# Optimization experiments

Measured on AMD Instinct MI355X. Metric: run time of the kernel, lower is better.

Reference implementation:

```python
import jax, jax.numpy as jnp
import numpy as np

B, S, H = 2, 2048, 1024
NH, HD = 16, 64
WIN = 256
EPS = 1e-5


def _layernorm(x, g, b):
    # normalize over last dim (head_dim)
    m = jnp.mean(x, axis=-1, keepdims=True)
    v = jnp.mean((x - m) ** 2, axis=-1, keepdims=True)
    return (x - m) * jax.lax.rsqrt(v + EPS) * g + b


def setup_inputs() -> dict:
    key = jax.random.key(0)
    ks = jax.random.split(key, 6)
    scale = 1.0 / np.sqrt(2.0 * H)  # ~ xavier_uniform with gain 1/sqrt(2)
    inp = {
        "x": jax.random.normal(ks[0], (B, S, H), dtype=jnp.float32),
        "Wq": jax.random.normal(ks[1], (H, H), dtype=jnp.float32) * scale,
        "bq": jnp.zeros((H,), jnp.float32),
        "Wk": jax.random.normal(ks[2], (H, H), dtype=jnp.float32) * scale,
        "bk": jnp.zeros((H,), jnp.float32),
        "Wv": jax.random.normal(ks[3], (H, H), dtype=jnp.float32) * scale,
        "bv": jnp.zeros((H,), jnp.float32),
        "Wo": jax.random.normal(ks[4], (H, H), dtype=jnp.float32) * scale,
        "bo": jnp.zeros((H,), jnp.float32),
        "ln_q_w": jnp.ones((HD,), jnp.float32),
        "ln_q_b": jnp.zeros((HD,), jnp.float32),
        "ln_k_w": jnp.ones((HD,), jnp.float32),
        "ln_k_b": jnp.zeros((HD,), jnp.float32),
    }
    return inp


def reference(x, Wq, bq, Wk, bk, Wv, bv, Wo, bo, ln_q_w, ln_q_b, ln_k_w, ln_k_b):
    b, s, _ = x.shape
    # projections (torch Linear: x @ W.T + b)
    q = (x @ Wq.T + bq).reshape(b, s, NH, HD)
    k = (x @ Wk.T + bk).reshape(b, s, NH, HD)
    v = (x @ Wv.T + bv).reshape(b, s, NH, HD)
    # QK layernorm over head_dim
    q = _layernorm(q, ln_q_w, ln_q_b)
    k = _layernorm(k, ln_k_w, ln_k_b)
    # scores [b, h, s, s]
    scores = jnp.einsum("bqhd,bkhd->bhqk", q, k) / np.sqrt(HD).astype(np.float32)
    i = jnp.arange(s)[:, None]
    j = jnp.arange(s)[None, :]
    mask = (j <= i) & (i - j <= WIN)
    scores = jnp.where(mask[None, None], scores, -jnp.inf)
    probs = jax.nn.softmax(scores, axis=-1)
    out = jnp.einsum("bhqk,bkhd->bqhd", probs, v).reshape(b, s, NH * HD)
    return out @ Wo.T + bo
```

## Files before the change

kernel.cpp:

```cpp
#include <hip/hip_runtime.h>
#include <hip/hip_bf16.h>
#include <cstdint>

typedef __hip_bfloat16 bf16;
typedef __attribute__((ext_vector_type(8))) short s16x8;
typedef __attribute__((ext_vector_type(4))) float f32x4;

#define NB_B 2
#define NB_S 2048
#define NB_H 1024
#define NB_NH 16
#define NB_HD 64
#define NB_WIN 256
#define NTOK 4096

static __device__ __forceinline__ unsigned pack_bf16(float a, float b) {
    bf16 ta = __float2bfloat16(a), tb = __float2bfloat16(b);
    return (unsigned)*(unsigned short*)&ta | ((unsigned)*(unsigned short*)&tb << 16);
}
static __device__ __forceinline__ unsigned short bf16u(float a) {
    bf16 t = __float2bfloat16(a);
    return *(unsigned short*)&t;
}

#define VMCNT(n) asm volatile("s_waitcnt vmcnt(" #n ")" ::: "memory")
#define SBAR __builtin_amdgcn_s_barrier()

__global__ void k_castall(const float* __restrict__ x, const float* __restrict__ Wq,
                          const float* __restrict__ Wk, const float* __restrict__ Wv,
                          const float* __restrict__ Wo,
                          bf16* __restrict__ xb, bf16* __restrict__ wqkvb,
                          bf16* __restrict__ wob) {
    int idx = blockIdx.x * blockDim.x + threadIdx.x;
    const float* in; bf16* out; int i;
    if (idx < 1048576)        { in = x;  out = xb;              i = idx * 4; }
    else if (idx < 1310720)   { in = Wq; out = wqkvb;           i = (idx - 1048576) * 4; }
    else if (idx < 1572864)   { in = Wk; out = wqkvb + 1048576; i = (idx - 1310720) * 4; }
    else if (idx < 1835008)   { in = Wv; out = wqkvb + 2097152; i = (idx - 1572864) * 4; }
    else                      { in = Wo; out = wob;             i = (idx - 1835008) * 4; }
    const float4 v = *(const float4*)(in + i);
    ushort4 u;
    u.x = bf16u(v.x); u.y = bf16u(v.y); u.z = bf16u(v.z); u.w = bf16u(v.w);
    *(ushort4*)((unsigned short*)out + i) = u;
}

#define G2_STAGE(AD, BD, KT)                                                         \
    do {                                                                             \
        _Pragma("unroll")                                                            \
        for (int it_ = 0; it_ < 4; ++it_) {                                          \
            int c_ = it_ * 512 + tid;                                                \
            int row_ = c_ >> 3, pc_ = c_ & 7;                                        \
            int col_ = ((pc_ ^ (row_ & 7)) << 3);                                    \
            __builtin_amdgcn_global_load_lds(                                        \
                (const __attribute__((address_space(1))) void*)(Ap + (size_t)(m0 + row_) * 1024 + (KT) + col_), \
                (__attribute__((address_space(3))) void*)((AD) + c_ * 8), 16, 0, 0); \
            __builtin_amdgcn_global_load_lds(                                        \
                (const __attribute__((address_space(1))) void*)(Bp + (size_t)(n0 + row_) * 1024 + (KT) + col_), \
                (__attribute__((address_space(3))) void*)((BD) + c_ * 8), 16, 0, 0); \
        }                                                                            \
        __builtin_amdgcn_sched_barrier(0);                                           \
    } while (0)

#define G2_COMPUTE(AS, BS)                                                           \
    do {                                                                             \
        _Pragma("unroll")                                                            \
        for (int kk_ = 0; kk_ < 2; ++kk_) {                                          \
            const int rchunk_ = (((kk_ << 2) + g) ^ (q & 7)) << 3;                   \
            s16x8 af_[8], bf_[4];                                                    \
            _Pragma("unroll")                                                        \
            for (int mi_ = 0; mi_ < 8; ++mi_)                                        \
                af_[mi_] = *(const s16x8*)&(AS)[(wr * 128 + mi_ * 16 + q) * 64 + rchunk_]; \
            _Pragma("unroll")                                                        \
            for (int ni_ = 0; ni_ < 4; ++ni_)                                        \
                bf_[ni_] = *(const s16x8*)&(BS)[(wc * 64 + ni_ * 16 + q) * 64 + rchunk_]; \
            __builtin_amdgcn_s_setprio(1);                                           \
            _Pragma("unroll")                                                        \
            for (int mi_ = 0; mi_ < 8; ++mi_)                                        \
                _Pragma("unroll")                                                    \
                for (int ni_ = 0; ni_ < 4; ++ni_)                                    \
                    acc[mi_][ni_] = __builtin_amdgcn_mfma_f32_16x16x32_bf16(         \
                        af_[mi_], bf_[ni_], acc[mi_][ni_], 0, 0, 0);                 \
            __builtin_amdgcn_s_setprio(0);                                           \
        }                                                                            \
    } while (0)

#define G2_MAINLOOP                                                                  \
    G2_STAGE(As0, Bs0, 0);                                                           \
    G2_STAGE(As1, Bs1, 64);                                                          \
    for (int i_ = 0; i_ < 7; ++i_) {                                                 \
        const int kt_ = i_ * 128;                                                    \
        VMCNT(8); SBAR;                                                              \
        G2_COMPUTE(As0, Bs0);                                                        \
        SBAR;                                                                        \
        G2_STAGE(As0, Bs0, kt_ + 128);                                               \
        VMCNT(8); SBAR;                                                              \
        G2_COMPUTE(As1, Bs1);                                                        \
        SBAR;                                                                        \
        G2_STAGE(As1, Bs1, kt_ + 192);                                               \
    }                                                                                \
    VMCNT(8); SBAR;                                                                  \
    G2_COMPUTE(As0, Bs0);                                                            \
    VMCNT(0); SBAR;                                                                  \
    G2_COMPUTE(As1, Bs1)

__global__ __launch_bounds__(512, 2) void k_gemm_qkv(const bf16* __restrict__ Ap,
                                                  const bf16* __restrict__ Bp,
                                                  const float* __restrict__ bq,
                                                  const float* __restrict__ bk,
                                                  const float* __restrict__ bv,
                                                  const float* __restrict__ lqw,
                                                  const float* __restrict__ lqb,
                                                  const float* __restrict__ lkw,
                                                  const float* __restrict__ lkb,
                                                  bf16* __restrict__ qbuf,
                                                  bf16* __restrict__ kbuf,
                                                  bf16* __restrict__ vtb) {
    __shared__ bf16 As0[256 * 64], As1[256 * 64];
    __shared__ bf16 Bs0[256 * 64], Bs1[256 * 64];
    const int tid = threadIdx.x;
    const int lane = tid & 63;
    const int wid = tid >> 6;
    const int wr = wid >> 2, wc = wid & 3;

    const int orig = blockIdx.y * gridDim.x + blockIdx.x;
    const int wk = (orig & 7) * 24 + (orig >> 3);
    const int m0 = (wk / 12) * 256, n0 = (wk % 12) * 256;

    const int g = lane >> 4, q = lane & 15;

    f32x4 acc[8][4] = {};

    G2_MAINLOOP;

    const int col0 = n0 + wc * 64;
    const int hh = col0 >> 6;
    const int csub = col0 & 1023;
    const float* bias = (hh < 16) ? bq : (hh < 32) ? bk : bv;

    float bcol[4];
#pragma unroll
    for (int ni = 0; ni < 4; ++ni) bcol[ni] = bias[csub + ni * 16 + q];
#pragma unroll
    for (int mi = 0; mi < 8; ++mi)
#pragma unroll
        for (int ni = 0; ni < 4; ++ni)
#pragma unroll
            for (int r = 0; r < 4; ++r) acc[mi][ni][r] += bcol[ni];

    if (hh < 32) {
        const float* gwa = (hh < 16) ? lqw : lkw;
        const float* gba = (hh < 16) ? lqb : lkb;
        float gam[4], bet[4];
#pragma unroll
        for (int ni = 0; ni < 4; ++ni) {
            gam[ni] = gwa[ni * 16 + q];
            bet[ni] = gba[ni * 16 + q];
        }
        bf16* outp = (hh < 16) ? qbuf : kbuf;
#pragma unroll
        for (int mi = 0; mi < 8; ++mi)
#pragma unroll
            for (int r = 0; r < 4; ++r) {
                float s1 = acc[mi][0][r] + acc[mi][1][r] + acc[mi][2][r] + acc[mi][3][r];
                float s2 = acc[mi][0][r] * acc[mi][0][r] + acc[mi][1][r] * acc[mi][1][r]
                         + acc[mi][2][r] * acc[mi][2][r] + acc[mi][3][r] * acc[mi][3][r];
#pragma unroll
                for (int mm = 1; mm < 16; mm <<= 1) {
                    s1 += __shfl_xor(s1, mm, 64);
                    s2 += __shfl_xor(s2, mm, 64);
                }
                float mean = s1 * (1.f / 64.f);
                float var = s2 * (1.f / 64.f) - mean * mean;
                float rs = rsqrtf(var + 1e-5f);
                int token = m0 + wr * 128 + mi * 16 + g * 4 + r;
#pragma unroll
                for (int ni = 0; ni < 4; ++ni) {
                    float y = (acc[mi][ni][r] - mean) * rs * gam[ni] + bet[ni];
                    outp[(size_t)token * 1024 + csub + ni * 16 + q] = __float2bfloat16(y);
                }
            }
    } else {
        const int b = m0 >> 11;
        const int bh = b * 16 + (csub >> 6);
        const int sbase0 = (m0 & 2047) + wr * 128 + g * 4;
#pragma unroll
        for (int mi = 0; mi < 8; ++mi) {
            const int sb = sbase0 + mi * 16;
#pragma unroll
            for (int ni = 0; ni < 4; ++ni) {
                const int d = ni * 16 + q;
                ushort4 u;
                u.x = bf16u(acc[mi][ni][0]); u.y = bf16u(acc[mi][ni][1]);
                u.z = bf16u(acc[mi][ni][2]); u.w = bf16u(acc[mi][ni][3]);
                *(ushort4*)(vtb + ((size_t)bh * 64 + d) * 2048 + sb) = u;
            }
        }
    }
}

#define G_STAGE(AD, BD, KT)                                                          \
    do {                                                                             \
        _Pragma("unroll")                                                            \
        for (int it_ = 0; it_ < 4; ++it_) {                                          \
            int c_ = it_ * 256 + tid;                                                \
            int row_ = c_ >> 3, pc_ = c_ & 7;                                        \
            int col_ = ((pc_ ^ (row_ & 7)) << 3);                                    \
            __builtin_amdgcn_global_load_lds(                                        \
                (const __attribute__((address_space(1))) void*)(Ap + (size_t)(m0 + row_) * 1024 + (KT) + col_), \
                (__attribute__((address_space(3))) void*)((AD) + c_ * 8), 16, 0, 0); \
            __builtin_amdgcn_global_load_lds(                                        \
                (const __attribute__((address_space(1))) void*)(Bp + (size_t)(n0 + row_) * 1024 + (KT) + col_), \
                (__attribute__((address_space(3))) void*)((BD) + c_ * 8), 16, 0, 0); \
        }                                                                            \
        __builtin_amdgcn_sched_barrier(0);                                           \
    } while (0)

#define G_COMPUTE(AS, BS)                                                            \
    do {                                                                             \
        _Pragma("unroll")                                                            \
        for (int kk_ = 0; kk_ < 2; ++kk_) {                                          \
            const int rchunk_ = (((kk_ << 2) + g) ^ (q & 7)) << 3;                   \
            s16x8 af_[4], bf_[4];                                                    \
            _Pragma("unroll")                                                        \
            for (int mi_ = 0; mi_ < 4; ++mi_)                                        \
                af_[mi_] = *(const s16x8*)&(AS)[(wr * 64 + mi_ * 16 + q) * 64 + rchunk_]; \
            _Pragma("unroll")                                                        \
            for (int ni_ = 0; ni_ < 4; ++ni_)                                        \
                bf_[ni_] = *(const s16x8*)&(BS)[(wc * 64 + ni_ * 16 + q) * 64 + rchunk_]; \
            __builtin_amdgcn_s_setprio(1);                                           \
            _Pragma("unroll")                                                        \
            for (int mi_ = 0; mi_ < 4; ++mi_)                                        \
                _Pragma("unroll")                                                    \
                for (int ni_ = 0; ni_ < 4; ++ni_)                                    \
                    acc[mi_][ni_] = __builtin_amdgcn_mfma_f32_16x16x32_bf16(         \
                        af_[mi_], bf_[ni_], acc[mi_][ni_], 0, 0, 0);                 \
            __builtin_amdgcn_s_setprio(0);                                           \
        }                                                                            \
    } while (0)

#define G_MAINLOOP                                                                   \
    G_STAGE(As0, Bs0, 0);                                                            \
    G_STAGE(As1, Bs1, 64);                                                           \
    for (int i_ = 0; i_ < 7; ++i_) {                                                 \
        const int kt_ = i_ * 128;                                                    \
        VMCNT(8); SBAR;                                                              \
        G_COMPUTE(As0, Bs0);                                                         \
        SBAR;                                                                        \
        G_STAGE(As0, Bs0, kt_ + 128);                                                \
        VMCNT(8); SBAR;                                                              \
        G_COMPUTE(As1, Bs1);                                                         \
        SBAR;                                                                        \
        G_STAGE(As1, Bs1, kt_ + 192);                                                \
    }                                                                                \
    VMCNT(8); SBAR;                                                                  \
    G_COMPUTE(As0, Bs0);                                                             \
    VMCNT(0); SBAR;                                                                  \
    G_COMPUTE(As1, Bs1)

__global__ __launch_bounds__(256) void k_gemm_out(const bf16* __restrict__ Ap,
                                                  const bf16* __restrict__ Bp,
                                                  const float* __restrict__ bias,
                                                  float* __restrict__ Cv) {
    __shared__ bf16 As0[128 * 64], As1[128 * 64];
    __shared__ bf16 Bs0[128 * 64], Bs1[128 * 64];
    const int tid = threadIdx.x;
    const int lane = tid & 63;
    const int w = tid >> 6;
    const int wr = w >> 1, wc = w & 1;

    const int orig = blockIdx.y * gridDim.x + blockIdx.x;
    const int wk = (orig & 7) * 32 + (orig >> 3);
    const int m0 = (wk / 8) * 128, n0 = (wk % 8) * 128;

    const int g = lane >> 4, q = lane & 15;

    f32x4 acc[4][4] = {};

    G_MAINLOOP;

#pragma unroll
    for (int mi = 0; mi < 4; ++mi)
#pragma unroll
        for (int ni = 0; ni < 4; ++ni) {
            int colg = n0 + wc * 64 + ni * 16 + q;
            float bcol = bias[colg];
#pragma unroll
            for (int r = 0; r < 4; ++r) {
                int rowg = m0 + wr * 64 + mi * 16 + g * 4 + r;
                Cv[(size_t)rowg * 1024 + colg] = acc[mi][ni][r] + bcol;
            }
        }
}

#undef G_STAGE
#undef G_COMPUTE
#undef G_MAINLOOP

__global__ __launch_bounds__(256) void k_attn(const bf16* __restrict__ qb,
                                              const bf16* __restrict__ kb,
                                              const bf16* __restrict__ vt,
                                              bf16* __restrict__ att) {
    __shared__ bf16 Ks[2][32 * 64];
    __shared__ bf16 Vs[2][64 * 32];

    const int orig = blockIdx.y * gridDim.x + blockIdx.x;
    const int wk = (orig & 7) * 128 + (orig >> 3);
    const int q0 = (wk & 31) * 64;
    const int bh = wk >> 5;

    const int b = bh >> 4, h = bh & 15;
    const int tid = threadIdx.x;
    const int w = tid >> 6;
    const int lane = tid & 63;
    const int g = lane >> 4, qi = lane & 15;
    const int qw0 = q0 + w * 16;
    const int iq = qw0 + qi;

    const size_t qbase = ((size_t)(b * 2048 + iq)) * 1024 + h * 64 + g * 8;
    s16x8 bq0 = *(const s16x8*)(qb + qbase);
    s16x8 bq1 = *(const s16x8*)(qb + qbase + 32);

    f32x4 o[4] = {};
    float lp = 0.f;

    int jmin = q0 - NB_WIN; if (jmin < 0) jmin = 0;
    const int c0 = jmin >> 5;
    const int c1 = (q0 + 63) >> 5;

    const int krow = tid >> 3, kpc = tid & 7;
    const int kcol = ((kpc ^ (krow & 7)) << 3);
    const int vrow = tid >> 2, vpc = tid & 3;
    const int vcol = ((vpc ^ (vrow & 3)) << 3);
    const bf16* kbase = kb + ((size_t)(b * 2048 + krow)) * 1024 + h * 64 + kcol;
    const bf16* vbase = vt + ((size_t)bh * 64 + vrow) * 2048 + vcol;

    __builtin_amdgcn_global_load_lds(
        (const __attribute__((address_space(1))) void*)(kbase + (size_t)(c0 * 32) * 1024),
        (__attribute__((address_space(3))) void*)(&Ks[0][tid * 8]), 16, 0, 0);
    __builtin_amdgcn_global_load_lds(
        (const __attribute__((address_space(1))) void*)(vbase + c0 * 32),
        (__attribute__((address_space(3))) void*)(&Vs[0][tid * 8]), 16, 0, 0);

    int buf = 0;
    for (int c = c0; c <= c1; ++c) {
        const int ks = c * 32;
        if (c < c1) {
            const int ksn = ks + 32;
            __builtin_amdgcn_global_load_lds(
                (const __attribute__((address_space(1))) void*)(kbase + (size_t)ksn * 1024),
                (__attribute__((address_space(3))) void*)(&Ks[buf ^ 1][tid * 8]), 16, 0, 0);
            __builtin_amdgcn_global_load_lds(
                (const __attribute__((address_space(1))) void*)(vbase + ksn),
                (__attribute__((address_space(3))) void*)(&Vs[buf ^ 1][tid * 8]), 16, 0, 0);
            __builtin_amdgcn_sched_barrier(0);
            VMCNT(2);
        } else {
            VMCNT(0);
        }
        SBAR;

        if (ks + 31 >= qw0 - NB_WIN && ks <= qw0 + 15) {
            const int ch0 = ((g ^ (qi & 7)) << 3);
            const bf16* kr0 = &Ks[buf][qi * 64];
            const bf16* kr1 = &Ks[buf][(16 + qi) * 64];
            s16x8 a00 = *(const s16x8*)(kr0 + ch0);
            s16x8 a01 = *(const s16x8*)(kr0 + (ch0 ^ 32));
            s16x8 a10 = *(const s16x8*)(kr1 + ch0);
            s16x8 a11 = *(const s16x8*)(kr1 + (ch0 ^ 32));

            f32x4 s0 = {}, s1 = {};
            s0 = __builtin_amdgcn_mfma_f32_16x16x32_bf16(a00, bq0, s0, 0, 0, 0);
            s0 = __builtin_amdgcn_mfma_f32_16x16x32_bf16(a01, bq1, s0, 0, 0, 0);
            s1 = __builtin_amdgcn_mfma_f32_16x16x32_bf16(a10, bq0, s1, 0, 0, 0);
            s1 = __builtin_amdgcn_mfma_f32_16x16x32_bf16(a11, bq1, s1, 0, 0, 0);

            float p0[4], p1[4];
#pragma unroll
            for (int r = 0; r < 4; ++r) {
                int j0 = ks + 4 * g + r, j1 = j0 + 16;
                p0[r] = ((unsigned)(iq - j0) <= (unsigned)NB_WIN)
                            ? __expf(s0[r] * 0.125f - 8.f) : 0.f;
                p1[r] = ((unsigned)(iq - j1) <= (unsigned)NB_WIN)
                            ? __expf(s1[r] * 0.125f - 8.f) : 0.f;
                lp += p0[r] + p1[r];
            }
            unsigned P0 = pack_bf16(p0[0], p0[1]), P1 = pack_bf16(p0[2], p0[3]);
            unsigned Q0 = pack_bf16(p1[0], p1[1]), Q1 = pack_bf16(p1[2], p1[3]);

            const int srcA = qi + (g & 1) * 32;
            const int srcB = srcA + 16;
            unsigned tP0a = __shfl((int)P0, srcA, 64), tQ0a = __shfl((int)Q0, srcA, 64);
            unsigned tP1a = __shfl((int)P1, srcA, 64), tQ1a = __shfl((int)Q1, srcA, 64);
            unsigned tP0b = __shfl((int)P0, srcB, 64), tQ0b = __shfl((int)Q0, srcB, 64);
            unsigned tP1b = __shfl((int)P1, srcB, 64), tQ1b = __shfl((int)Q1, srcB, 64);
            union { s16x8 v; unsigned u[4]; } pa;
            pa.u[0] = (g < 2) ? tP0a : tQ0a;
            pa.u[1] = (g < 2) ? tP1a : tQ1a;
            pa.u[2] = (g < 2) ? tP0b : tQ0b;
            pa.u[3] = (g < 2) ? tP1b : tQ1b;

            const int chv = ((g ^ (qi & 3)) << 3);
#pragma unroll
            for (int db = 0; db < 4; ++db) {
                s16x8 bv = *(const s16x8*)&Vs[buf][(db * 16 + qi) * 32 + chv];
                o[db] = __builtin_amdgcn_mfma_f32_16x16x32_bf16(pa.v, bv, o[db], 0, 0, 0);
            }
        }

        SBAR;
        buf ^= 1;
    }

    float l2 = lp + __shfl_xor(lp, 16, 64);
    float lf = l2 + __shfl_xor(l2, 32, 64);
    float lr[4];
#pragma unroll
    for (int r = 0; r < 4; ++r) lr[r] = __shfl(lf, 4 * g + r, 64);

#pragma unroll
    for (int db = 0; db < 4; ++db)
#pragma unroll
        for (int r = 0; r < 4; ++r) {
            float vlu = o[db][r] / lr[r];
            att[((size_t)(b * 2048 + qw0 + 4 * g + r)) * 1024 + h * 64 + db * 16 + qi] =
                __float2bfloat16(vlu);
        }
}

extern "C" void kernel_launch(void* const* d_in, const int* in_sizes, int n_in,
                              void* d_out, int out_size, void* d_ws, size_t ws_size,
                              hipStream_t stream) {
    const float* x   = (const float*)d_in[0];
    const float* Wq  = (const float*)d_in[1];
    const float* bq  = (const float*)d_in[2];
    const float* Wk  = (const float*)d_in[3];
    const float* bk  = (const float*)d_in[4];
    const float* Wv  = (const float*)d_in[5];
    const float* bv  = (const float*)d_in[6];
    const float* Wo  = (const float*)d_in[7];
    const float* bo  = (const float*)d_in[8];
    const float* lqw = (const float*)d_in[9];
    const float* lqb = (const float*)d_in[10];
    const float* lkw = (const float*)d_in[11];
    const float* lkb = (const float*)d_in[12];

    char* ws = (char*)d_ws;
    bf16* xb    = (bf16*)(ws + 0);
    bf16* wqkvb = (bf16*)(ws + 8388608);
    bf16* wob   = (bf16*)(ws + 14680064);
    bf16* qbuf  = (bf16*)(ws + 16777216);
    bf16* kbuf  = (bf16*)(ws + 25165824);
    bf16* vtb   = (bf16*)(ws + 33554432);
    bf16* attb  = (bf16*)(ws + 41943040);

    k_castall<<<8192, 256, 0, stream>>>(x, Wq, Wk, Wv, Wo, xb, wqkvb, wob);

    k_gemm_qkv<<<dim3(12, 16), 512, 0, stream>>>(xb, wqkvb, bq, bk, bv,
                                                 lqw, lqb, lkw, lkb,
                                                 qbuf, kbuf, vtb);

    k_attn<<<dim3(32, 32), 256, 0, stream>>>(qbuf, kbuf, vtb, attb);

    k_gemm_out<<<dim3(8, 32), 256, 0, stream>>>(attb, wob, bo, (float*)d_out);
}
```

Baseline: 90.43 us.

## Restructure QKV GEMM mainloop into phased LDS reads interleaved with MFMA

Replaces the two-stage prefetch mainloop of the QKV projection GEMM with a per-tile schedule. Each tile issues the global-to-LDS loads for the next tile up front, then splits its MFMA work into four phases. In each phase the wave reads a small slice of A from LDS, waits on lgkmcnt, and runs the MFMAs for that slice. The goal is to cut register pressure from holding all A fragments at once and to overlap LDS reads with MFMA, in the style of ping-pong scheduling. In exchange it adds more barriers, waits vmcnt(0) at the end of every tile, and effectively drops the prefetch depth from two stages to one.

Result: slower. 95.04 us (+5.1%).

```diff
diff --git a/kernel.cpp b/kernel.cpp
--- a/kernel.cpp
+++ b/kernel.cpp
@@ -25,6 +25,8 @@
 
 #define VMCNT(n) asm volatile("s_waitcnt vmcnt(" #n ")" ::: "memory")
 #define SBAR __builtin_amdgcn_s_barrier()
+#define LGKM0 do { asm volatile("s_waitcnt lgkmcnt(0)" ::: "memory"); \
+                   __builtin_amdgcn_sched_barrier(0); } while (0)
 
 __global__ void k_castall(const float* __restrict__ x, const float* __restrict__ Wq,
                           const float* __restrict__ Wk, const float* __restrict__ Wv,
@@ -61,47 +63,45 @@
         __builtin_amdgcn_sched_barrier(0);                                           \
     } while (0)
 
-#define G2_COMPUTE(AS, BS)                                                           \
-    do {                                                                             \
-        _Pragma("unroll")                                                            \
-        for (int kk_ = 0; kk_ < 2; ++kk_) {                                          \
-            const int rchunk_ = (((kk_ << 2) + g) ^ (q & 7)) << 3;                   \
-            s16x8 af_[8], bf_[4];                                                    \
-            _Pragma("unroll")                                                        \
-            for (int mi_ = 0; mi_ < 8; ++mi_)                                        \
-                af_[mi_] = *(const s16x8*)&(AS)[(wr * 128 + mi_ * 16 + q) * 64 + rchunk_]; \
+#define G2_READS_A(AS, P)                                                            \
+    _Pragma("unroll")                                                                \
+    for (int j_ = 0; j_ < 2; ++j_)                                                   \
+        _Pragma("unroll")                                                            \
+        for (int kk_ = 0; kk_ < 2; ++kk_)                                            \
+            af_[j_][kk_] = *(const s16x8*)&(AS)[(wr * 128 + ((P) * 2 + j_) * 16 + q) * 64 \
+                                                + ((((kk_ << 2) + g) ^ (q & 7)) << 3)];
+
+#define G2_MFMA(P)                                                                   \
+    __builtin_amdgcn_s_setprio(1);                                                   \
+    _Pragma("unroll")                                                                \
+    for (int kk_ = 0; kk_ < 2; ++kk_)                                                \
+        _Pragma("unroll")                                                            \
+        for (int j_ = 0; j_ < 2; ++j_)                                               \
             _Pragma("unroll")                                                        \
             for (int ni_ = 0; ni_ < 4; ++ni_)                                        \
-                bf_[ni_] = *(const s16x8*)&(BS)[(wc * 64 + ni_ * 16 + q) * 64 + rchunk_]; \
-            __builtin_amdgcn_s_setprio(1);                                           \
+                acc[(P) * 2 + j_][ni_] = __builtin_amdgcn_mfma_f32_16x16x32_bf16(    \
+                    af_[j_][kk_], bf_[ni_][kk_], acc[(P) * 2 + j_][ni_], 0, 0, 0);   \
+    __builtin_amdgcn_s_setprio(0);
+
+#define G2_TILE(AS, BS, AN, BN_, KTN)                                                \
+    do {                                                                             \
+        s16x8 af_[2][2], bf_[4][2];                                                  \
+        G2_READS_A(AS, 0);                                                           \
+        _Pragma("unroll")                                                            \
+        for (int ni_ = 0; ni_ < 4; ++ni_)                                            \
             _Pragma("unroll")                                                        \
-            for (int mi_ = 0; mi_ < 8; ++mi_)                                        \
-                _Pragma("unroll")                                                    \
-                for (int ni_ = 0; ni_ < 4; ++ni_)                                    \
-                    acc[mi_][ni_] = __builtin_amdgcn_mfma_f32_16x16x32_bf16(         \
-                        af_[mi_], bf_[ni_], acc[mi_][ni_], 0, 0, 0);                 \
-            __builtin_amdgcn_s_setprio(0);                                           \
-        }                                                                            \
+            for (int kk_ = 0; kk_ < 2; ++kk_)                                        \
+                bf_[ni_][kk_] = *(const s16x8*)&(BS)[(wc * 64 + ni_ * 16 + q) * 64   \
+                                                     + ((((kk_ << 2) + g) ^ (q & 7)) << 3)]; \
+        if ((KTN) < 1024) { G2_STAGE(AN, BN_, KTN); }                                \
+        SBAR; LGKM0;                                                                 \
+        G2_MFMA(0);                                                                  \
+        SBAR;                                                                        \
+        G2_READS_A(AS, 1); SBAR; LGKM0; G2_MFMA(1); SBAR;                            \
+        G2_READS_A(AS, 2); SBAR; LGKM0; G2_MFMA(2); SBAR;                            \
+        G2_READS_A(AS, 3); SBAR; LGKM0; G2_MFMA(3);                                  \
+        VMCNT(0); SBAR;                                                              \
     } while (0)
-
-#define G2_MAINLOOP                                                                  \
-    G2_STAGE(As0, Bs0, 0);                                                           \
-    G2_STAGE(As1, Bs1, 64);                                                          \
-    for (int i_ = 0; i_ < 7; ++i_) {                                                 \
-        const int kt_ = i_ * 128;                                                    \
-        VMCNT(8); SBAR;                                                              \
-        G2_COMPUTE(As0, Bs0);                                                        \
-        SBAR;                                                                        \
-        G2_STAGE(As0, Bs0, kt_ + 128);                                               \
-        VMCNT(8); SBAR;                                                              \
-        G2_COMPUTE(As1, Bs1);                                                        \
-        SBAR;                                                                        \
-        G2_STAGE(As1, Bs1, kt_ + 192);                                               \
-    }                                                                                \
-    VMCNT(8); SBAR;                                                                  \
-    G2_COMPUTE(As0, Bs0);                                                            \
-    VMCNT(0); SBAR;                                                                  \
-    G2_COMPUTE(As1, Bs1)
 
 __global__ __launch_bounds__(512, 2) void k_gemm_qkv(const bf16* __restrict__ Ap,
                                                   const bf16* __restrict__ Bp,
@@ -130,7 +130,14 @@
 
     f32x4 acc[8][4] = {};
 
-    G2_MAINLOOP;
+    G2_STAGE(As0, Bs0, 0);
+    VMCNT(0); SBAR;
+
+#pragma unroll 1
+    for (int t = 0; t < 16; t += 2) {
+        G2_TILE(As0, Bs0, As1, Bs1, t * 64 + 64);
+        G2_TILE(As1, Bs1, As0, Bs0, t * 64 + 128);
+    }
 
     const int col0 = n0 + wc * 64;
     const int hh = col0 >> 6;
```
